# Kernel optimization log

Hardware: AMD Instinct MI355X
Metric: run time of the kernel (lower is better)

The kernel has to match this reference:

```python
import jax, jax.numpy as jnp
import numpy as np

B, N, D = 4, 4096, 6
HID = 128
K = 16
NEG_SLOPE = 0.2


def _w(key, shape, fan_in):
    return jax.random.normal(key, shape, jnp.float32) / np.sqrt(fan_in)


def setup_inputs() -> dict:
    key = jax.random.key(0)
    ks = jax.random.split(key, 24)
    inp = {
        "x": jax.random.normal(ks[0], (B, N, D), jnp.float32),
        # conv1: GATConv(D, 64, heads=4) -> 256
        "W1": _w(ks[1], (D, 256), D),
        "a_src1": _w(ks[2], (4, 64), 64),
        "a_dst1": _w(ks[3], (4, 64), 64),
        "b1": jnp.zeros((256,), jnp.float32),
        # conv2: GATConv(256, 64, heads=4) -> 256
        "W2": _w(ks[4], (256, 256), 256),
        "a_src2": _w(ks[5], (4, 64), 64),
        "a_dst2": _w(ks[6], (4, 64), 64),
        "b2": jnp.zeros((256,), jnp.float32),
        # conv3: GATConv(256, 128, heads=1) -> 128
        "W3": _w(ks[7], (256, 128), 256),
        "a_src3": _w(ks[8], (1, 128), 128),
        "a_dst3": _w(ks[9], (1, 128), 128),
        "b3": jnp.zeros((128,), jnp.float32),
        # residual Linear(D, HID)
        "res_W": _w(ks[10], (D, HID), D),
        "res_b": jnp.zeros((HID,), jnp.float32),
        # MLP: HID -> HID -> HID//2 -> D
        "m1_W": _w(ks[11], (HID, HID), HID),
        "m1_b": jnp.zeros((HID,), jnp.float32),
        "m2_W": _w(ks[12], (HID, HID // 2), HID),
        "m2_b": jnp.zeros((HID // 2,), jnp.float32),
        "m3_W": _w(ks[13], (HID // 2, D), HID // 2),
        "m3_b": jnp.zeros((D,), jnp.float32),
    }
    return inp


def knn_edges(x, k):
    """x: [B,N,d] -> (src, dst) int32 edge lists (flow source->target),
    per-batch kNN (loop=False) followed by self-loop append (GATConv default)."""
    b, n, _ = x.shape
    sq = jnp.sum(x * x, axis=-1)  # [B,N]
    d2 = sq[:, :, None] + sq[:, None, :] - 2.0 * jnp.einsum('bnd,bmd->bnm', x, x)
    d2 = jnp.where(jnp.eye(n, dtype=bool)[None], jnp.inf, d2)
    _, idx = jax.lax.top_k(-d2, k)  # [B,N,k] neighbor (source) indices
    offs = (jnp.arange(b, dtype=jnp.int32) * n)[:, None, None]
    src = (idx.astype(jnp.int32) + offs).reshape(-1)
    dst = (jnp.broadcast_to(jnp.arange(n, dtype=jnp.int32)[None, :, None], (b, n, k)) + offs).reshape(-1)
    loops = jnp.arange(b * n, dtype=jnp.int32)
    return jnp.concatenate([src, loops]), jnp.concatenate([dst, loops])


def gat_layer(x, src, dst, W, a_src, a_dst, bias, heads, n_nodes):
    c = a_src.shape[-1]
    h = (x @ W).reshape(n_nodes, heads, c)          # [N,H,C]
    al_s = jnp.sum(h * a_src[None], axis=-1)        # [N,H]
    al_d = jnp.sum(h * a_dst[None], axis=-1)        # [N,H]
    e = jax.nn.leaky_relu(al_s[src] + al_d[dst], NEG_SLOPE)  # [E,H]
    m = jax.ops.segment_max(e, dst, num_segments=n_nodes)
    ee = jnp.exp(e - m[dst])
    den = jax.ops.segment_sum(ee, dst, num_segments=n_nodes)
    alpha = ee / den[dst]                            # [E,H] softmax over incoming edges
    out = jax.ops.segment_sum(alpha[:, :, None] * h[src], dst, num_segments=n_nodes)
    return out.reshape(n_nodes, heads * c) + bias


def _gelu(v):
    return jax.nn.gelu(v, approximate=False)


def reference(x, W1, a_src1, a_dst1, b1, W2, a_src2, a_dst2, b2,
              W3, a_src3, a_dst3, b3, res_W, res_b,
              m1_W, m1_b, m2_W, m2_b, m3_W, m3_b):
    b, n, d = x.shape
    nn_tot = b * n
    x_flat = x.reshape(nn_tot, d)
    src, dst = knn_edges(x, K)
    y = _gelu(gat_layer(x_flat, src, dst, W1, a_src1, a_dst1, b1, 4, nn_tot))
    y = _gelu(gat_layer(y, src, dst, W2, a_src2, a_dst2, b2, 4, nn_tot))
    y = _gelu(gat_layer(y, src, dst, W3, a_src3, a_dst3, b3, 1, nn_tot))
    y = y + x_flat @ res_W + res_b
    y = _gelu(y @ m1_W + m1_b)
    y = _gelu(y @ m2_W + m2_b)
    y = y @ m3_W + m3_b
    return y.reshape(b, n, -1)
```

## Files before the change

kernel.cpp:

```cpp
#include <hip/hip_runtime.h>
#include <math.h>

#define NN 16384
#define NPB 4096
#define KCAP 128
#define TS 512
#define GUARD 0.25f

typedef __attribute__((ext_vector_type(8))) short short8v;
typedef __attribute__((ext_vector_type(4))) float float4v;
typedef __attribute__((ext_vector_type(2))) _Float16 half2v;

#if defined(__has_builtin)
#if __has_builtin(__builtin_amdgcn_fdot2)
#define HAS_FDOT2 1
#endif
#endif

#ifdef HAS_FDOT2
#define FDOT2(a,b,c) __builtin_amdgcn_fdot2((a),(b),(c),false)
#else
__device__ __forceinline__ float FDOT2(half2v a, half2v b, float c){
  return c + (float)a[0]*(float)b[0] + (float)a[1]*(float)b[1];
}
#endif

__device__ __forceinline__ float gelu_f(float v){
  return 0.5f*v*(1.0f+erff(v*0.70710678118654752440f));
}

__device__ __forceinline__ unsigned short f2bf(float v){
  union{float f; unsigned u;} c; c.f = v;
  const unsigned r = c.u + 0x7FFFu + ((c.u >> 16) & 1u);
  return (unsigned short)(r >> 16);
}
__device__ __forceinline__ float bf2f(unsigned short b){
  return __uint_as_float(((unsigned)b) << 16);
}

__device__ __forceinline__ unsigned fmap(float d2){
  unsigned u = __float_as_uint(d2);
  return u ^ ((unsigned)((int)u >> 31) | 0x80000000u);
}

__device__ __forceinline__ unsigned dkey(const float4 qa, const float4 qb, const float sqn,
                                         const float4 a, const float4 b){
  const float dot = qa.x*a.x + qa.y*a.y + qa.z*a.z + qa.w*a.w + qb.x*b.x + qb.y*b.y;
  const float d2 = sqn + b.z - 2.0f*dot;
  return fmap(d2);
}

__device__ __forceinline__ unsigned long long bsort64(unsigned long long v, int lane){
#pragma unroll
  for (int k=2;k<=64;k<<=1){
#pragma unroll
    for (int j=k>>1;j>0;j>>=1){
      const unsigned long long o = __shfl_xor(v, j);
      const bool keepMin = ((lane & k) == 0) == ((lane & j) == 0);
      const unsigned long long mn = v < o ? v : o;
      const unsigned long long mx = v < o ? o : v;
      v = keepMin ? mn : mx;
    }
  }
  return v;
}

__device__ __forceinline__ unsigned bsort32(unsigned v, int lane){
#pragma unroll
  for (int k=2;k<=64;k<<=1){
#pragma unroll
    for (int j=k>>1;j>0;j>>=1){
      const unsigned o = __shfl_xor(v, j);
      const bool keepMin = ((lane & k) == 0) == ((lane & j) == 0);
      const unsigned mn = v < o ? v : o;
      const unsigned mx = v < o ? o : v;
      v = keepMin ? mn : mx;
    }
  }
  return v;
}

__global__ __launch_bounds__(256) void prep_k(const float* __restrict__ x,
                                              float4* __restrict__ PA, float4* __restrict__ PB,
                                              uint4* __restrict__ PH,
                                              const float* __restrict__ W2, const float* __restrict__ W3,
                                              const float* __restrict__ m1W, const float* __restrict__ m2W,
                                              unsigned short* __restrict__ o){
  if (blockIdx.x < NN/256){
    const int n = blockIdx.x*256 + threadIdx.x;
    const float* xr = x + (size_t)n*6;
    const float x0=xr[0],x1=xr[1],x2=xr[2],x3=xr[3],x4=xr[4],x5=xr[5];
    const float sq = x0*x0+x1*x1+x2*x2+x3*x3+x4*x4+x5*x5;
    PA[n] = make_float4(x0,x1,x2,x3);
    PB[n] = make_float4(x4,x5,sq,0.f);
    half2v h01 = {(_Float16)x0, (_Float16)x1};
    half2v h23 = {(_Float16)x2, (_Float16)x3};
    half2v h45 = {(_Float16)x4, (_Float16)x5};
    uint4 ph;
    ph.x = __builtin_bit_cast(unsigned, h01);
    ph.y = __builtin_bit_cast(unsigned, h23);
    ph.z = __builtin_bit_cast(unsigned, h45);
    ph.w = __float_as_uint(sq);
    PH[n] = ph;
  } else {
    const int i = (blockIdx.x - NN/256)*256 + threadIdx.x;
    float v;
    if (i < 65536)       v = W2[i];
    else if (i < 98304)  v = W3[i-65536];
    else if (i < 114688) v = m1W[i-98304];
    else                 v = m2W[i-114688];
    o[i] = f2bf(v);
  }
}

__global__ void knn_k(const uint4* __restrict__ PH, const float4* __restrict__ PA,
                      const float4* __restrict__ PB, int* __restrict__ nbr){
  __shared__ uint2 C1[2][TS];
  __shared__ uint2 C2[2][TS];
  __shared__ unsigned skey[4][KCAP];
  __shared__ unsigned sslot[4][KCAP];
  const int t = threadIdx.x, w = t >> 6, lane = t & 63;
  const int n = blockIdx.x*4 + w;
  const int base = n & ~(NPB-1);
  const uint4 qh = PH[n];
  const half2v q01 = __builtin_bit_cast(half2v, qh.x);
  const half2v q23 = __builtin_bit_cast(half2v, qh.y);
  const half2v q45 = __builtin_bit_cast(half2v, qh.z);
  const float sqn = __uint_as_float(qh.w);
  const int selfslot = n - base;

  {
    const uint4 c0 = PH[base + t];
    const uint4 c1 = PH[base + 256 + t];
    C1[0][t]     = make_uint2(c0.x, c0.y);
    C2[0][t]     = make_uint2(c0.z, c0.w);
    C1[0][256+t] = make_uint2(c1.x, c1.y);
    C2[0][256+t] = make_uint2(c1.z, c1.w);
  }
  __syncthreads();

  unsigned kp[32];
  float minf = 3e38f;
#pragma unroll
  for (int tile=0; tile<NPB/TS; ++tile){
    const int buf = tile & 1;
    uint4 n0, n1;
    if (tile < NPB/TS-1){
      n0 = PH[base + (tile+1)*TS + t];
      n1 = PH[base + (tile+1)*TS + 256 + t];
    }
    unsigned lo = 0;
#pragma unroll
    for (int it=0; it<TS/64; ++it){
      const int s = it*64 + lane;
      const uint2 c1 = C1[buf][s];
      const uint2 c2 = C2[buf][s];
      const float dot = FDOT2(q01, __builtin_bit_cast(half2v, c1.x),
                        FDOT2(q23, __builtin_bit_cast(half2v, c1.y),
                        FDOT2(q45, __builtin_bit_cast(half2v, c2.x), 0.f)));
      float d2 = fmaf(-2.f, dot, sqn + __uint_as_float(c2.y));
      d2 = fmaxf(d2, 0.f);
      if (tile*TS + s == selfslot) d2 = 3e38f;
      minf = fminf(minf, d2);
      const unsigned u16 = __float_as_uint(d2) >> 16;
      if ((it & 1) == 0) lo = u16;
      else               kp[(tile*(TS/64)+it)>>1] = lo | (u16 << 16);
    }
    if (tile < NPB/TS-1){
      C1[buf^1][t]     = make_uint2(n0.x, n0.y);
      C2[buf^1][t]     = make_uint2(n0.z, n0.w);
      C1[buf^1][256+t] = make_uint2(n1.x, n1.y);
      C2[buf^1][256+t] = make_uint2(n1.z, n1.w);
      __syncthreads();
    }
  }

  unsigned T = bsort32(__float_as_uint(minf), lane);
  T = __shfl(T, 15);
  const float TG = __uint_as_float(T) + GUARD;
  const unsigned T16 = __float_as_uint(TG) >> 16;

  int cnt = 0;
#pragma unroll
  for (int q=0; q<64; ++q){
    const unsigned k16 = (kp[q>>1] >> ((q&1)*16)) & 0xFFFFu;
    const bool p = k16 <= T16;
    const unsigned long long bb = __ballot(p);
    if (p){
      const int pos = cnt + (int)__popcll(bb & ((1ull << lane) - 1ull));
      if (pos < KCAP) sslot[w][pos] = (unsigned)((q>>3)*TS + (q&7)*64 + lane);
    }
    cnt += (int)__popcll(bb);
  }
  if (cnt > KCAP) cnt = KCAP;

  for (int i=lane; i<cnt; i+=64){
    const int slot = (int)sslot[w][i];
    const float4 qa = PA[n];
    const float4 qb = PB[n];
    skey[w][i] = dkey(qa, qb, qb.z, PA[base+slot], PB[base+slot]);
  }

  unsigned long long vbest;
  {
    unsigned long long v = ~0ull;
    if (lane < cnt) v = ((unsigned long long)skey[w][lane] << 32) | sslot[w][lane];
    vbest = bsort64(v, lane);
  }
  for (int c=1; c*64 < cnt; ++c){
    const int i = c*64 + lane;
    unsigned long long v = ~0ull;
    if (i < cnt) v = ((unsigned long long)skey[w][i] << 32) | sslot[w][i];
    v = bsort64(v, lane);
    const unsigned long long r = __shfl(v, 63-lane);
    vbest = vbest < r ? vbest : r;
#pragma unroll
    for (int j=32;j>0;j>>=1){
      const unsigned long long o = __shfl_xor(vbest, j);
      const bool keepMin = (lane & j) == 0;
      const unsigned long long mn = vbest < o ? vbest : o;
      const unsigned long long mx = vbest < o ? o : vbest;
      vbest = keepMin ? mn : mx;
    }
  }
  if (lane < 16) nbr[n*16 + lane] = base + (int)(vbest & 0xFFFFFFFFull);
}

__global__ __launch_bounds__(256) void gemm_in6(const float* __restrict__ x, const float* __restrict__ W,
                                                const float* __restrict__ asrc, const float* __restrict__ adst,
                                                unsigned short* __restrict__ h,
                                                float* __restrict__ als, float* __restrict__ ald){
  const int t = blockIdx.x*256 + threadIdx.x;
  const int n = t >> 6, cg = t & 63;
  const float* xr = x + n*6;
  float xv[6];
#pragma unroll
  for (int d=0; d<6; d++) xv[d] = xr[d];
  float4 acc = make_float4(0.f,0.f,0.f,0.f);
#pragma unroll
  for (int d=0; d<6; d++){
    const float4 wv = *(const float4*)(W + d*256 + cg*4);
    acc.x += xv[d]*wv.x; acc.y += xv[d]*wv.y; acc.z += xv[d]*wv.z; acc.w += xv[d]*wv.w;
  }
  ushort4 o;
  o.x = f2bf(acc.x); o.y = f2bf(acc.y); o.z = f2bf(acc.z); o.w = f2bf(acc.w);
  *(ushort4*)(h + (size_t)n*256 + cg*4) = o;

  const int head = cg >> 4;
  const float4 av = *(const float4*)(asrc + head*64 + (cg&15)*4);
  const float4 dv = *(const float4*)(adst + head*64 + (cg&15)*4);
  float s = acc.x*av.x + acc.y*av.y + acc.z*av.z + acc.w*av.w;
  float d = acc.x*dv.x + acc.y*dv.y + acc.z*dv.z + acc.w*dv.w;
#pragma unroll
  for (int off=1; off<16; off<<=1){
    s += __shfl_xor(s, off);
    d += __shfl_xor(d, off);
  }
  if ((cg & 15) == 0){
    als[n*4 + head] = s;
    ald[n*4 + head] = d;
  }
}

template<int HEADS, int C, bool RES, bool ALSPLIT>
__global__ __launch_bounds__(256) void agg_k(const unsigned short* __restrict__ h,
                                             const float* __restrict__ als, const float* __restrict__ ald,
                                             const int* __restrict__ nbr,
                                             const float* __restrict__ bias, unsigned short* __restrict__ out,
                                             const float* __restrict__ xin, const float* __restrict__ rW,
                                             const float* __restrict__ rb){
  constexpr int CT = HEADS*C;
  constexpr int F  = CT/64;
  const int bid = blockIdx.x;
  const int sbid = (bid & 7)*512 + (bid >> 3);
  const int w = threadIdx.x >> 6, lane = threadIdx.x & 63;
  const int n = sbid*4 + w;
  const int head = (lane*F)/C;
  const int col  = lane*F;
  const int nb = nbr[n*16 + (lane & 15)];
  float aldn;
  if constexpr (ALSPLIT) aldn = ald[n*2] + ald[n*2+1];
  else                   aldn = ald[n*HEADS + head];
  float e[17];
#pragma unroll
  for (int j=0;j<17;j++){
    const int sj = (j<16) ? __shfl(nb, j) : n;
    float v;
    if constexpr (ALSPLIT) v = als[sj*2] + als[sj*2+1] + aldn;
    else                   v = als[sj*HEADS + head] + aldn;
    e[j] = v > 0.f ? v : 0.2f*v;
  }
  float mx = e[0];
#pragma unroll
  for (int j=1;j<17;j++) mx = fmaxf(mx, e[j]);
  float den = 0.f;
#pragma unroll
  for (int j=0;j<17;j++){ e[j] = expf(e[j]-mx); den += e[j]; }
  float acc[F];
#pragma unroll
  for (int f=0;f<F;f++) acc[f]=0.f;
#pragma unroll
  for (int j=0;j<17;j++){
    const int sj = (j<16) ? __shfl(nb, j) : n;
    const unsigned short* hp = h + (size_t)sj*CT + col;
    if constexpr (F==4){
      const ushort4 v = *(const ushort4*)hp;
      acc[0] += e[j]*bf2f(v.x); acc[1] += e[j]*bf2f(v.y);
      acc[2] += e[j]*bf2f(v.z); acc[3] += e[j]*bf2f(v.w);
    } else {
      const ushort2 v = *(const ushort2*)hp;
      acc[0] += e[j]*bf2f(v.x); acc[1] += e[j]*bf2f(v.y);
    }
  }
  const float inv = 1.f/den;
  if constexpr (F==4){
    ushort4 o;
    o.x = f2bf(gelu_f(acc[0]*inv + bias[col+0]));
    o.y = f2bf(gelu_f(acc[1]*inv + bias[col+1]));
    o.z = f2bf(gelu_f(acc[2]*inv + bias[col+2]));
    o.w = f2bf(gelu_f(acc[3]*inv + bias[col+3]));
    *(ushort4*)(out + (size_t)n*CT + col) = o;
  } else {
    float v0 = gelu_f(acc[0]*inv + bias[col+0]);
    float v1 = gelu_f(acc[1]*inv + bias[col+1]);
    if constexpr (RES){
      const float* xr = xin + (size_t)n*6;
      float r0 = rb[col+0], r1 = rb[col+1];
#pragma unroll
      for (int d=0; d<6; d++){
        const float xv = xr[d];
        r0 += xv*rW[d*128 + col+0];
        r1 += xv*rW[d*128 + col+1];
      }
      v0 += r0; v1 += r1;
    }
    ushort2 o;
    o.x = f2bf(v0); o.y = f2bf(v1);
    *(ushort2*)(out + (size_t)n*CT + col) = o;
  }
}

template<int KC, int NC, bool BIAS, bool GELU, bool OUTBF16, bool AL, int ALH>
__global__ __launch_bounds__(256) void mgemm_k(const unsigned short* __restrict__ A,
                                               const unsigned short* __restrict__ B,
                                               const float* __restrict__ bias, void* __restrict__ Cout,
                                               const float* __restrict__ asrc, const float* __restrict__ adst,
                                               float* __restrict__ als, float* __restrict__ ald){
  __shared__ unsigned short As[4*128*8];
  __shared__ unsigned short Bs[4*64*8];
  const int t = threadIdx.x, wid = t >> 6, lane = t & 63;
  const int r0 = blockIdx.x*128, c0 = blockIdx.y*64;
  const int lg = lane >> 4, l15 = lane & 15;
  float4v acc[2][4];
#pragma unroll
  for (int rf=0;rf<2;rf++)
#pragma unroll
    for (int cf=0;cf<4;cf++)
#pragma unroll
      for (int r=0;r<4;r++) acc[rf][cf][r] = 0.f;

  const int arow = t >> 1, ak0 = (t & 1)*16;
  const int bk = t >> 3, bn0 = (t & 7)*8;

#pragma unroll 1
  for (int kc=0; kc<KC; kc+=32){
    __syncthreads();
    const unsigned short* Ap = A + (size_t)(r0+arow)*KC + kc + ak0;
    const short8v av0 = *(const short8v*)Ap;
    const short8v av1 = *(const short8v*)(Ap + 8);
    *(short8v*)&As[((ak0>>3)+0)*1024 + arow*8] = av0;
    *(short8v*)&As[((ak0>>3)+1)*1024 + arow*8] = av1;
    const unsigned short* Bp = B + (size_t)(kc+bk)*NC + c0 + bn0;
    const short8v bv = *(const short8v*)Bp;
#pragma unroll
    for (int i=0;i<8;i++) Bs[(bk>>3)*512 + (bn0+i)*8 + (bk&7)] = (unsigned short)bv[i];
    __syncthreads();

    short8v af0 = *(const short8v*)&As[lg*1024 + (wid*32 +  0 + l15)*8];
    short8v af1 = *(const short8v*)&As[lg*1024 + (wid*32 + 16 + l15)*8];
    short8v bf[4];
#pragma unroll
    for (int c=0;c<4;c++) bf[c] = *(const short8v*)&Bs[lg*512 + (c*16 + l15)*8];
#pragma unroll
    for (int cf=0;cf<4;cf++){
      acc[0][cf] = __builtin_amdgcn_mfma_f32_16x16x32_bf16(af0, bf[cf], acc[0][cf], 0,0,0);
      acc[1][cf] = __builtin_amdgcn_mfma_f32_16x16x32_bf16(af1, bf[cf], acc[1][cf], 0,0,0);
    }
  }

  float av[4], dv[4];
  if constexpr (AL){
#pragma unroll
    for (int cf=0;cf<4;cf++){
      av[cf] = asrc[c0 + cf*16 + l15];
      dv[cf] = adst[c0 + cf*16 + l15];
    }
  }
#pragma unroll
  for (int rf=0;rf<2;rf++)
#pragma unroll
    for (int r=0;r<4;r++){
      const int row = r0 + wid*32 + rf*16 + lg*4 + r;
      float s = 0.f, d = 0.f;
#pragma unroll
      for (int cf=0;cf<4;cf++){
        const int col = c0 + cf*16 + l15;
        float v = acc[rf][cf][r];
        if constexpr (BIAS) v += bias[col];
        if constexpr (GELU) v = gelu_f(v);
        if constexpr (OUTBF16) ((unsigned short*)Cout)[(size_t)row*NC + col] = f2bf(v);
        else                   ((float*)Cout)[(size_t)row*NC + col] = v;
        if constexpr (AL){ s += v*av[cf]; d += v*dv[cf]; }
      }
      if constexpr (AL){
#pragma unroll
        for (int off=1; off<16; off<<=1){
          s += __shfl_xor(s, off);
          d += __shfl_xor(d, off);
        }
        if (l15 == 0){
          als[row*ALH + (c0>>6)] = s;
          ald[row*ALH + (c0>>6)] = d;
        }
      }
    }
}

__global__ __launch_bounds__(256) void m3_k(const unsigned short* __restrict__ A, const float* __restrict__ W,
                                            const float* __restrict__ bias, float* __restrict__ out){
  __shared__ float Wl[64*6];
  __shared__ float bl[6];
  const int t = threadIdx.x;
  for (int i=t; i<384; i+=256) Wl[i] = W[i];
  if (t < 6) bl[t] = bias[t];
  __syncthreads();
  const int n = blockIdx.x*256 + t;
  const unsigned short* ap = A + (size_t)n*64;
  float acc[6] = {0.f,0.f,0.f,0.f,0.f,0.f};
  for (int k=0;k<64;k+=8){
    const short8v v = *(const short8v*)(ap+k);
#pragma unroll
    for (int u=0;u<8;u++){
      const float f = bf2f((unsigned short)v[u]);
#pragma unroll
      for (int j=0;j<6;j++)
        acc[j] += f*Wl[(k+u)*6+j];
    }
  }
#pragma unroll
  for (int j=0;j<6;j++) out[n*6+j] = acc[j] + bl[j];
}

extern "C" void kernel_launch(void* const* d_in, const int* in_sizes, int n_in,
                              void* d_out, int out_size, void* d_ws, size_t ws_size,
                              hipStream_t stream){
  (void)in_sizes; (void)n_in; (void)out_size; (void)ws_size;
  const float* x      = (const float*)d_in[0];
  const float* W1     = (const float*)d_in[1];
  const float* a_src1 = (const float*)d_in[2];
  const float* a_dst1 = (const float*)d_in[3];
  const float* b1     = (const float*)d_in[4];
  const float* W2     = (const float*)d_in[5];
  const float* a_src2 = (const float*)d_in[6];
  const float* a_dst2 = (const float*)d_in[7];
  const float* b2     = (const float*)d_in[8];
  const float* W3     = (const float*)d_in[9];
  const float* a_src3 = (const float*)d_in[10];
  const float* a_dst3 = (const float*)d_in[11];
  const float* b3     = (const float*)d_in[12];
  const float* res_W  = (const float*)d_in[13];
  const float* res_b  = (const float*)d_in[14];
  const float* m1_W   = (const float*)d_in[15];
  const float* m1_b   = (const float*)d_in[16];
  const float* m2_W   = (const float*)d_in[17];
  const float* m2_b   = (const float*)d_in[18];
  const float* m3_W   = (const float*)d_in[19];
  const float* m3_b   = (const float*)d_in[20];
  float* out = (float*)d_out;

  char* wsb = (char*)d_ws;
  int*            nbr   = (int*)wsb;
  unsigned short* HB256 = (unsigned short*)(wsb + (1u<<20));
  unsigned short* YB256 = (unsigned short*)(wsb + (9u<<20));
  unsigned short* HB128 = (unsigned short*)(wsb + (17u<<20));
  unsigned short* YB128 = (unsigned short*)(wsb + (21u<<20));
  unsigned short* HM128 = (unsigned short*)(wsb + (25u<<20));
  unsigned short* Y64   = (unsigned short*)(wsb + (29u<<20));
  float*          ALS   = (float*)(wsb + (31u<<20));
  float*          ALD   = ALS + NN*4;
  float4*         PA    = (float4*)(wsb + (31u<<20) + (512u<<10));
  float4*         PB    = PA + NN;
  uint4*          PH    = (uint4*)(wsb + (32u<<20));
  unsigned short* Wb    = (unsigned short*)(wsb + (32u<<20) + (512u<<10));
  unsigned short* W2b = Wb;
  unsigned short* W3b = Wb + 65536;
  unsigned short* m1b = Wb + 98304;
  unsigned short* m2b = Wb + 114688;

  prep_k<<<NN/256 + 480, 256, 0, stream>>>(x, PA, PB, PH, W2, W3, m1_W, m2_W, Wb);
  knn_k<<<NN/4, 256, 0, stream>>>(PH, PA, PB, nbr);

  gemm_in6<<<NN/4, 256, 0, stream>>>(x, W1, a_src1, a_dst1, HB256, ALS, ALD);
  agg_k<4,64,false,false><<<NN/4, 256, 0, stream>>>(HB256, ALS, ALD, nbr, b1, YB256, nullptr, nullptr, nullptr);

  mgemm_k<256,256,false,false,true,true,4><<<dim3(128,4), 256, 0, stream>>>(
      YB256, W2b, nullptr, HB256, a_src2, a_dst2, ALS, ALD);
  agg_k<4,64,false,false><<<NN/4, 256, 0, stream>>>(HB256, ALS, ALD, nbr, b2, YB256, nullptr, nullptr, nullptr);

  mgemm_k<256,128,false,false,true,true,2><<<dim3(128,2), 256, 0, stream>>>(
      YB256, W3b, nullptr, HB128, a_src3, a_dst3, ALS, ALD);
  agg_k<1,128,true,true><<<NN/4, 256, 0, stream>>>(HB128, ALS, ALD, nbr, b3, YB128, x, res_W, res_b);

  mgemm_k<128,128,true,true,true,false,1><<<dim3(128,2), 256, 0, stream>>>(
      YB128, m1b, m1_b, HM128, nullptr, nullptr, nullptr, nullptr);
  mgemm_k<128,64,true,true,true,false,1><<<dim3(128,1), 256, 0, stream>>>(
      HM128, m2b, m2_b, Y64, nullptr, nullptr, nullptr, nullptr);
  m3_k<<<NN/256, 256, 0, stream>>>(Y64, m3_W, m3_b, out);
}
```

Baseline: 177.4 us.

## Merge kNN with layer-1 projection and fuse MLP layer 2 with output layer

The layer-1 input projection (gemm_in6) now runs inside the kNN kernel: odd blocks compute the projection and even blocks do the kNN search, so the two independent jobs share one launch and can overlap. A new mlp2_k kernel computes the m2 GEMM with MFMA, applies bias and GELU, and then performs the 64->6 m3 projection in registers using shuffle reductions. This removes the Y64 intermediate buffer round trip and two kernel launches. The risk is that the combined kernel uses the kNN kernel's shared-memory allocation for projection blocks too, which may lower occupancy, and that mlp2_k runs only 128 blocks.

```diff
diff --git a/kernel.cpp b/kernel.cpp
--- a/kernel.cpp
+++ b/kernel.cpp
@@ -113,14 +113,53 @@
   }
 }
 
-__global__ void knn_k(const uint4* __restrict__ PH, const float4* __restrict__ PA,
-                      const float4* __restrict__ PB, int* __restrict__ nbr){
+__global__ void kng_k(const uint4* __restrict__ PH, const float4* __restrict__ PA,
+                      const float4* __restrict__ PB, int* __restrict__ nbr,
+                      const float* __restrict__ x, const float* __restrict__ W1,
+                      const float* __restrict__ asrc, const float* __restrict__ adst,
+                      unsigned short* __restrict__ h,
+                      float* __restrict__ als, float* __restrict__ ald){
   __shared__ uint2 C1[2][TS];
   __shared__ uint2 C2[2][TS];
   __shared__ unsigned skey[4][KCAP];
   __shared__ unsigned sslot[4][KCAP];
+
+  if (blockIdx.x & 1){
+    const int t = (blockIdx.x >> 1)*256 + threadIdx.x;
+    const int n = t >> 6, cg = t & 63;
+    const float* xr = x + n*6;
+    float xv[6];
+#pragma unroll
+    for (int d=0; d<6; d++) xv[d] = xr[d];
+    float4 acc = make_float4(0.f,0.f,0.f,0.f);
+#pragma unroll
+    for (int d=0; d<6; d++){
+      const float4 wv = *(const float4*)(W1 + d*256 + cg*4);
+      acc.x += xv[d]*wv.x; acc.y += xv[d]*wv.y; acc.z += xv[d]*wv.z; acc.w += xv[d]*wv.w;
+    }
+    ushort4 o;
+    o.x = f2bf(acc.x); o.y = f2bf(acc.y); o.z = f2bf(acc.z); o.w = f2bf(acc.w);
+    *(ushort4*)(h + (size_t)n*256 + cg*4) = o;
+
+    const int head = cg >> 4;
+    const float4 av = *(const float4*)(asrc + head*64 + (cg&15)*4);
+    const float4 dv = *(const float4*)(adst + head*64 + (cg&15)*4);
+    float s = acc.x*av.x + acc.y*av.y + acc.z*av.z + acc.w*av.w;
+    float d = acc.x*dv.x + acc.y*dv.y + acc.z*dv.z + acc.w*dv.w;
+#pragma unroll
+    for (int off=1; off<16; off<<=1){
+      s += __shfl_xor(s, off);
+      d += __shfl_xor(d, off);
+    }
+    if ((cg & 15) == 0){
+      als[n*4 + head] = s;
+      ald[n*4 + head] = d;
+    }
+    return;
+  }
+
   const int t = threadIdx.x, w = t >> 6, lane = t & 63;
-  const int n = blockIdx.x*4 + w;
+  const int n = (blockIdx.x >> 1)*4 + w;
   const int base = n & ~(NPB-1);
   const uint4 qh = PH[n];
   const half2v q01 = __builtin_bit_cast(half2v, qh.x);
@@ -224,42 +263,6 @@
     }
   }
   if (lane < 16) nbr[n*16 + lane] = base + (int)(vbest & 0xFFFFFFFFull);
-}
-
-__global__ __launch_bounds__(256) void gemm_in6(const float* __restrict__ x, const float* __restrict__ W,
-                                                const float* __restrict__ asrc, const float* __restrict__ adst,
-                                                unsigned short* __restrict__ h,
-                                                float* __restrict__ als, float* __restrict__ ald){
-  const int t = blockIdx.x*256 + threadIdx.x;
-  const int n = t >> 6, cg = t & 63;
-  const float* xr = x + n*6;
-  float xv[6];
-#pragma unroll
-  for (int d=0; d<6; d++) xv[d] = xr[d];
-  float4 acc = make_float4(0.f,0.f,0.f,0.f);
-#pragma unroll
-  for (int d=0; d<6; d++){
-    const float4 wv = *(const float4*)(W + d*256 + cg*4);
-    acc.x += xv[d]*wv.x; acc.y += xv[d]*wv.y; acc.z += xv[d]*wv.z; acc.w += xv[d]*wv.w;
-  }
-  ushort4 o;
-  o.x = f2bf(acc.x); o.y = f2bf(acc.y); o.z = f2bf(acc.z); o.w = f2bf(acc.w);
-  *(ushort4*)(h + (size_t)n*256 + cg*4) = o;
-
-  const int head = cg >> 4;
-  const float4 av = *(const float4*)(asrc + head*64 + (cg&15)*4);
-  const float4 dv = *(const float4*)(adst + head*64 + (cg&15)*4);
-  float s = acc.x*av.x + acc.y*av.y + acc.z*av.z + acc.w*av.w;
-  float d = acc.x*dv.x + acc.y*dv.y + acc.z*dv.z + acc.w*dv.w;
-#pragma unroll
-  for (int off=1; off<16; off<<=1){
-    s += __shfl_xor(s, off);
-    d += __shfl_xor(d, off);
-  }
-  if ((cg & 15) == 0){
-    als[n*4 + head] = s;
-    ald[n*4 + head] = d;
-  }
 }
 
 template<int HEADS, int C, bool RES, bool ALSPLIT>
@@ -426,29 +429,84 @@
     }
 }
 
-__global__ __launch_bounds__(256) void m3_k(const unsigned short* __restrict__ A, const float* __restrict__ W,
-                                            const float* __restrict__ bias, float* __restrict__ out){
-  __shared__ float Wl[64*6];
-  __shared__ float bl[6];
-  const int t = threadIdx.x;
-  for (int i=t; i<384; i+=256) Wl[i] = W[i];
-  if (t < 6) bl[t] = bias[t];
-  __syncthreads();
-  const int n = blockIdx.x*256 + t;
-  const unsigned short* ap = A + (size_t)n*64;
-  float acc[6] = {0.f,0.f,0.f,0.f,0.f,0.f};
-  for (int k=0;k<64;k+=8){
-    const short8v v = *(const short8v*)(ap+k);
-#pragma unroll
-    for (int u=0;u<8;u++){
-      const float f = bf2f((unsigned short)v[u]);
-#pragma unroll
-      for (int j=0;j<6;j++)
-        acc[j] += f*Wl[(k+u)*6+j];
-    }
-  }
-#pragma unroll
-  for (int j=0;j<6;j++) out[n*6+j] = acc[j] + bl[j];
+__global__ __launch_bounds__(256) void mlp2_k(const unsigned short* __restrict__ A,
+                                              const unsigned short* __restrict__ B,
+                                              const float* __restrict__ bias2,
+                                              const float* __restrict__ W3, const float* __restrict__ b3,
+                                              float* __restrict__ out){
+  __shared__ unsigned short As[4*128*8];
+  __shared__ unsigned short Bs[4*64*8];
+  const int t = threadIdx.x, wid = t >> 6, lane = t & 63;
+  const int r0 = blockIdx.x*128;
+  const int lg = lane >> 4, l15 = lane & 15;
+  float4v acc[2][4];
+#pragma unroll
+  for (int rf=0;rf<2;rf++)
+#pragma unroll
+    for (int cf=0;cf<4;cf++)
+#pragma unroll
+      for (int r=0;r<4;r++) acc[rf][cf][r] = 0.f;
+
+  const int arow = t >> 1, ak0 = (t & 1)*16;
+  const int bk = t >> 3, bn0 = (t & 7)*8;
+
+#pragma unroll 1
+  for (int kc=0; kc<128; kc+=32){
+    __syncthreads();
+    const unsigned short* Ap = A + (size_t)(r0+arow)*128 + kc + ak0;
+    const short8v av0 = *(const short8v*)Ap;
+    const short8v av1 = *(const short8v*)(Ap + 8);
+    *(short8v*)&As[((ak0>>3)+0)*1024 + arow*8] = av0;
+    *(short8v*)&As[((ak0>>3)+1)*1024 + arow*8] = av1;
+    const unsigned short* Bp = B + (size_t)(kc+bk)*64 + bn0;
+    const short8v bv = *(const short8v*)Bp;
+#pragma unroll
+    for (int i=0;i<8;i++) Bs[(bk>>3)*512 + (bn0+i)*8 + (bk&7)] = (unsigned short)bv[i];
+    __syncthreads();
+
+    short8v af0 = *(const short8v*)&As[lg*1024 + (wid*32 +  0 + l15)*8];
+    short8v af1 = *(const short8v*)&As[lg*1024 + (wid*32 + 16 + l15)*8];
+    short8v bf[4];
+#pragma unroll
+    for (int c=0;c<4;c++) bf[c] = *(const short8v*)&Bs[lg*512 + (c*16 + l15)*8];
+#pragma unroll
+    for (int cf=0;cf<4;cf++){
+      acc[0][cf] = __builtin_amdgcn_mfma_f32_16x16x32_bf16(af0, bf[cf], acc[0][cf], 0,0,0);
+      acc[1][cf] = __builtin_amdgcn_mfma_f32_16x16x32_bf16(af1, bf[cf], acc[1][cf], 0,0,0);
+    }
+  }
+
+  float w3[4][6];
+#pragma unroll
+  for (int cf=0;cf<4;cf++)
+#pragma unroll
+    for (int j=0;j<6;j++) w3[cf][j] = W3[(cf*16 + l15)*6 + j];
+  float b2l[4];
+#pragma unroll
+  for (int cf=0;cf<4;cf++) b2l[cf] = bias2[cf*16 + l15];
+
+#pragma unroll
+  for (int rf=0;rf<2;rf++)
+#pragma unroll
+    for (int r=0;r<4;r++){
+      const int row = r0 + wid*32 + rf*16 + lg*4 + r;
+      float p[6] = {0.f,0.f,0.f,0.f,0.f,0.f};
+#pragma unroll
+      for (int cf=0;cf<4;cf++){
+        float v = gelu_f(acc[rf][cf][r] + b2l[cf]);
+        const float vv = bf2f(f2bf(v));
+#pragma unroll
+        for (int j=0;j<6;j++) p[j] += vv*w3[cf][j];
+      }
+#pragma unroll
+      for (int off=1; off<16; off<<=1)
+#pragma unroll
+        for (int j=0;j<6;j++) p[j] += __shfl_xor(p[j], off);
+      if (l15 == 0){
+#pragma unroll
+        for (int j=0;j<6;j++) out[(size_t)row*6 + j] = p[j] + b3[j];
+      }
+    }
 }
 
 extern "C" void kernel_launch(void* const* d_in, const int* in_sizes, int n_in,
@@ -485,7 +543,6 @@
   unsigned short* HB128 = (unsigned short*)(wsb + (17u<<20));
   unsigned short* YB128 = (unsigned short*)(wsb + (21u<<20));
   unsigned short* HM128 = (unsigned short*)(wsb + (25u<<20));
-  unsigned short* Y64   = (unsigned short*)(wsb + (29u<<20));
   float*          ALS   = (float*)(wsb + (31u<<20));
   float*          ALD   = ALS + NN*4;
   float4*         PA    = (float4*)(wsb + (31u<<20) + (512u<<10));
@@ -498,9 +555,8 @@
   unsigned short* m2b = Wb + 114688;
 
   prep_k<<<NN/256 + 480, 256, 0, stream>>>(x, PA, PB, PH, W2, W3, m1_W, m2_W, Wb);
-  knn_k<<<NN/4, 256, 0, stream>>>(PH, PA, PB, nbr);
-
-  gemm_in6<<<NN/4, 256, 0, stream>>>(x, W1, a_src1, a_dst1, HB256, ALS, ALD);
+
+  kng_k<<<NN/2, 256, 0, stream>>>(PH, PA, PB, nbr, x, W1, a_src1, a_dst1, HB256, ALS, ALD);
   agg_k<4,64,false,false><<<NN/4, 256, 0, stream>>>(HB256, ALS, ALD, nbr, b1, YB256, nullptr, nullptr, nullptr);
 
   mgemm_k<256,256,false,false,true,true,4><<<dim3(128,4), 256, 0, stream>>>(
@@ -513,7 +569,5 @@
 
   mgemm_k<128,128,true,true,true,false,1><<<dim3(128,2), 256, 0, stream>>>(
       YB128, m1b, m1_b, HM128, nullptr, nullptr, nullptr, nullptr);
-  mgemm_k<128,64,true,true,true,false,1><<<dim3(128,1), 256, 0, stream>>>(
-      HM128, m2b, m2_b, Y64, nullptr, nullptr, nullptr, nullptr);
-  m3_k<<<NN/256, 256, 0, stream>>>(Y64, m3_W, m3_b, out);
-}
+  mlp2_k<<<128, 256, 0, stream>>>(HM128, m2b, m2_b, m3_W, m3_b, out);
+}
```

Result: slower. 212.2 us (+19.6%).
